# Optimization experiments

Measured on AMD Instinct MI355X. Metric: run time of the kernel, lower is better.

The kernel has to match this reference:

```python
import jax, jax.numpy as jnp
import numpy as np

NUM_POINTS = 2048
FEAT_DIMS = 512
BATCH = 32


def setup_inputs() -> dict:
    key = jax.random.key(0)
    ks = jax.random.split(key, 7)
    glf = jax.random.normal(ks[0], (BATCH, FEAT_DIMS, 1), dtype=jnp.float32)
    # Per-position linear weights (one Conv1d(k=1) per position, fused):
    # W[p, out, in], b[p, out]. Scale like PyTorch Conv1d default init.
    W1 = jax.random.normal(ks[1], (NUM_POINTS, 32, FEAT_DIMS), dtype=jnp.float32) * (1.0 / np.sqrt(FEAT_DIMS))
    b1 = jax.random.normal(ks[2], (NUM_POINTS, 32), dtype=jnp.float32) * 0.01
    W2 = jax.random.normal(ks[3], (NUM_POINTS, 8, 32), dtype=jnp.float32) * (1.0 / np.sqrt(32))
    b2 = jax.random.normal(ks[4], (NUM_POINTS, 8), dtype=jnp.float32) * 0.01
    W3 = jax.random.normal(ks[5], (NUM_POINTS, 3, 8), dtype=jnp.float32) * (1.0 / np.sqrt(8))
    b3 = jax.random.normal(ks[6], (NUM_POINTS, 3), dtype=jnp.float32) * 0.01
    return {"glf": glf, "W1": W1, "b1": b1, "W2": W2, "b2": b2, "W3": W3, "b3": b3}


def _fc_layer(x, W, b):
    # x: [B, Cin, P], W: [P, Cout, Cin], b: [P, Cout] -> [B, Cout, P]
    return jnp.einsum('bip,poi->bop', x, W) + b.T[None, :, :]


def reference(glf, W1, b1, W2, b2, W3, b3):
    # glf: [B, feat_dims, 1] -> repeat along positions
    x = jnp.broadcast_to(glf, (glf.shape[0], glf.shape[1], NUM_POINTS))
    x = _fc_layer(x, W1, b1)  # [B, 32, P]
    x = _fc_layer(x, W2, b2)  # [B, 8, P]
    x = _fc_layer(x, W3, b3)  # [B, 3, P]  (seg_class == 0)
    return x
```

## Files before the change

### kernel.cpp

```cpp
#include <hip/hip_runtime.h>

#define NUM_POINTS 2048
#define FEAT 512
#define BATCH 32
#define POS_PER_BLOCK 2

using v8s = __attribute__((ext_vector_type(8))) short;
using v4f = __attribute__((ext_vector_type(4))) float;

static __device__ __forceinline__ short f2bf(float x) {
  unsigned u = __float_as_uint(x);
  u += 0x7FFFu + ((u >> 16) & 1u);
  return (short)(u >> 16);
}

__global__ void __launch_bounds__(256, 2) fcdec_fused(
    const float* __restrict__ glf,
    const float* __restrict__ W1, const float* __restrict__ b1,
    const float* __restrict__ W2, const float* __restrict__ b2,
    const float* __restrict__ W3, const float* __restrict__ b3,
    float* __restrict__ out) {
  __shared__ char smem[32768];
  short* bfrag = (short*)smem;
  float (*h1s)[32][33] = (float (*)[32][33])smem;

  const int t = threadIdx.x;
  const int w = t >> 6;
  const int l = t & 63;
  const int lp = w >> 1;
  const int mt = w & 1;
  const int p = blockIdx.x * POS_PER_BLOCK + lp;
  const int lrow = l & 15;
  const int lk = (l >> 4) << 3;

  float4 g[16];
  #pragma unroll
  for (int rep = 0; rep < 16; ++rep) {
    const int c = rep * 256 + t;
    const int b = c >> 7;
    const int k0 = (c & 127) << 2;
    g[rep] = *(const float4*)(glf + b * FEAT + k0);
  }

  const float* A0 = W1 + ((size_t)p * 32u + mt * 16 + lrow) * FEAT + lk;
  float4 fa[16], fb[16];
  #pragma unroll
  for (int ks = 0; ks < 16; ++ks) {
    fa[ks] = *(const float4*)(A0 + ks * 32);
    fb[ks] = *(const float4*)(A0 + ks * 32 + 4);
  }

  #pragma unroll
  for (int rep = 0; rep < 16; ++rep) {
    const int c = rep * 256 + t;
    const int b = c >> 7;
    const int k0 = (c & 127) << 2;
    const int ks = k0 >> 5;
    const int gsel = (k0 >> 3) & 3;
    const int j0 = k0 & 7;
    const int nt = b >> 4;
    const int ll = gsel * 16 + (b & 15);
    short* dst = bfrag + (((ks * 2 + nt) * 64 + ll) << 3) + j0;
    dst[0] = f2bf(g[rep].x); dst[1] = f2bf(g[rep].y);
    dst[2] = f2bf(g[rep].z); dst[3] = f2bf(g[rep].w);
  }
  __syncthreads();

  v4f acc0 = {}, acc1 = {};
  #pragma unroll
  for (int ks = 0; ks < 16; ++ks) {
    v8s a;
    a[0] = f2bf(fa[ks].x); a[1] = f2bf(fa[ks].y);
    a[2] = f2bf(fa[ks].z); a[3] = f2bf(fa[ks].w);
    a[4] = f2bf(fb[ks].x); a[5] = f2bf(fb[ks].y);
    a[6] = f2bf(fb[ks].z); a[7] = f2bf(fb[ks].w);
    v8s bv0 = *(const v8s*)(bfrag + (((ks * 2 + 0) * 64 + l) << 3));
    v8s bv1 = *(const v8s*)(bfrag + (((ks * 2 + 1) * 64 + l) << 3));
    acc0 = __builtin_amdgcn_mfma_f32_16x16x32_bf16(a, bv0, acc0, 0, 0, 0);
    acc1 = __builtin_amdgcn_mfma_f32_16x16x32_bf16(a, bv1, acc1, 0, 0, 0);
  }

  __syncthreads();

  #pragma unroll
  for (int r = 0; r < 4; ++r) {
    const int o = mt * 16 + ((l >> 4) << 2) + r;
    const float bb = b1[p * 32 + o];
    h1s[lp][o][lrow] = acc0[r] + bb;
    h1s[lp][o][16 + lrow] = acc1[r] + bb;
  }
  __syncthreads();

  if (t < POS_PER_BLOCK * BATCH) {
    const int tp = t >> 5;
    const int b = t & 31;
    const int pg = blockIdx.x * POS_PER_BLOCK + tp;
    float h2[8];
    #pragma unroll
    for (int o8 = 0; o8 < 8; ++o8) {
      float s = b2[pg * 8 + o8];
      const float* w2 = W2 + (size_t)(pg * 8 + o8) * 32;
      #pragma unroll
      for (int i = 0; i < 32; ++i) s += w2[i] * h1s[tp][i][b];
      h2[o8] = s;
    }
    #pragma unroll
    for (int c = 0; c < 3; ++c) {
      float s = b3[pg * 3 + c];
      const float* w3 = W3 + (size_t)(pg * 3 + c) * 8;
      #pragma unroll
      for (int j = 0; j < 8; ++j) s += w3[j] * h2[j];
      out[(size_t)(b * 3 + c) * NUM_POINTS + pg] = s;
    }
  }
}

extern "C" void kernel_launch(void* const* d_in, const int* in_sizes, int n_in,
                              void* d_out, int out_size, void* d_ws, size_t ws_size,
                              hipStream_t stream) {
  const float* glf = (const float*)d_in[0];
  const float* W1  = (const float*)d_in[1];
  const float* b1  = (const float*)d_in[2];
  const float* W2  = (const float*)d_in[3];
  const float* b2  = (const float*)d_in[4];
  const float* W3  = (const float*)d_in[5];
  const float* b3  = (const float*)d_in[6];
  float* out = (float*)d_out;

  hipLaunchKernelGGL(fcdec_fused, dim3(NUM_POINTS / POS_PER_BLOCK), dim3(256), 0, stream,
                     glf, W1, b1, W2, b2, W3, b3, out);
}
```

Measured before the change: 35.86 us.

## Halve W1 register prefetch with rolling reload, truncate-pack bf16, raise occupancy

Switches fp32-to-bf16 conversion from round-to-nearest-even to truncation, using one v_perm per pair of values, and packs the LDS stores of the glf fragment into 8-byte writes. The W1 prefetch buffer shrinks from 16 to 8 float4 pairs per lane, and the second half is reloaded into the freed slots inside the MFMA loop. Launch bounds are raised from 2 to 3 blocks per SIMD. The aim is fewer conversion ALU ops, lower register pressure and higher occupancy to hide the memory-bound W1 stream. Truncation adds a small extra rounding error, and the second half of the loads is exposed with less prefetch distance.

```diff
diff --git a/kernel.cpp b/kernel.cpp
--- a/kernel.cpp
+++ b/kernel.cpp
@@ -6,15 +6,14 @@
 #define POS_PER_BLOCK 2
 
 using v8s = __attribute__((ext_vector_type(8))) short;
+using v4u = __attribute__((ext_vector_type(4))) unsigned;
 using v4f = __attribute__((ext_vector_type(4))) float;
 
-static __device__ __forceinline__ short f2bf(float x) {
-  unsigned u = __float_as_uint(x);
-  u += 0x7FFFu + ((u >> 16) & 1u);
-  return (short)(u >> 16);
+static __device__ __forceinline__ unsigned pk_trunc(float x, float y) {
+  return __builtin_amdgcn_perm(__float_as_uint(y), __float_as_uint(x), 0x07060302u);
 }
 
-__global__ void __launch_bounds__(256, 2) fcdec_fused(
+__global__ void __launch_bounds__(256, 3) fcdec_fused(
     const float* __restrict__ glf,
     const float* __restrict__ W1, const float* __restrict__ b1,
     const float* __restrict__ W2, const float* __restrict__ b2,
@@ -43,11 +42,11 @@
   }
 
   const float* A0 = W1 + ((size_t)p * 32u + mt * 16 + lrow) * FEAT + lk;
-  float4 fa[16], fb[16];
+  float4 fa[8], fb[8];
   #pragma unroll
-  for (int ks = 0; ks < 16; ++ks) {
-    fa[ks] = *(const float4*)(A0 + ks * 32);
-    fb[ks] = *(const float4*)(A0 + ks * 32 + 4);
+  for (int kk = 0; kk < 8; ++kk) {
+    fa[kk] = *(const float4*)(A0 + kk * 32);
+    fb[kk] = *(const float4*)(A0 + kk * 32 + 4);
   }
 
   #pragma unroll
@@ -60,22 +59,30 @@
     const int j0 = k0 & 7;
     const int nt = b >> 4;
     const int ll = gsel * 16 + (b & 15);
-    short* dst = bfrag + (((ks * 2 + nt) * 64 + ll) << 3) + j0;
-    dst[0] = f2bf(g[rep].x); dst[1] = f2bf(g[rep].y);
-    dst[2] = f2bf(g[rep].z); dst[3] = f2bf(g[rep].w);
+    uint2 pk;
+    pk.x = pk_trunc(g[rep].x, g[rep].y);
+    pk.y = pk_trunc(g[rep].z, g[rep].w);
+    *(uint2*)(bfrag + (((ks * 2 + nt) * 64 + ll) << 3) + j0) = pk;
   }
   __syncthreads();
 
   v4f acc0 = {}, acc1 = {};
   #pragma unroll
   for (int ks = 0; ks < 16; ++ks) {
-    v8s a;
-    a[0] = f2bf(fa[ks].x); a[1] = f2bf(fa[ks].y);
-    a[2] = f2bf(fa[ks].z); a[3] = f2bf(fa[ks].w);
-    a[4] = f2bf(fb[ks].x); a[5] = f2bf(fb[ks].y);
-    a[6] = f2bf(fb[ks].z); a[7] = f2bf(fb[ks].w);
-    v8s bv0 = *(const v8s*)(bfrag + (((ks * 2 + 0) * 64 + l) << 3));
-    v8s bv1 = *(const v8s*)(bfrag + (((ks * 2 + 1) * 64 + l) << 3));
+    const float4 c0 = fa[ks & 7];
+    const float4 c1 = fb[ks & 7];
+    if (ks < 8) {
+      fa[ks] = *(const float4*)(A0 + (ks + 8) * 32);
+      fb[ks] = *(const float4*)(A0 + (ks + 8) * 32 + 4);
+    }
+    v4u au;
+    au[0] = pk_trunc(c0.x, c0.y);
+    au[1] = pk_trunc(c0.z, c0.w);
+    au[2] = pk_trunc(c1.x, c1.y);
+    au[3] = pk_trunc(c1.z, c1.w);
+    const v8s a = __builtin_bit_cast(v8s, au);
+    const v8s bv0 = *(const v8s*)(bfrag + (((ks * 2 + 0) * 64 + l) << 3));
+    const v8s bv1 = *(const v8s*)(bfrag + (((ks * 2 + 1) * 64 + l) << 3));
     acc0 = __builtin_amdgcn_mfma_f32_16x16x32_bf16(a, bv0, acc0, 0, 0, 0);
     acc1 = __builtin_amdgcn_mfma_f32_16x16x32_bf16(a, bv1, acc1, 0, 0, 0);
   }
```

New measurement: 31.76 us. 11.4% less time.
